# Performance work log

Hardware: AMD Instinct MI355X
Metric: run time of the kernel (lower is better)

Reference implementation:

```python
import jax, jax.numpy as jnp
import numpy as np

B, D, NT, NZ = 16384, 64, 128, 2048


def setup_inputs() -> dict:
    key = jax.random.key(0)
    ks = jax.random.split(key, 5)
    return {
        "t": jax.random.uniform(ks[0], (1,), dtype=jnp.float32),
        "z": jax.random.normal(ks[1], (B, D), dtype=jnp.float32),
        "logp_z": jnp.zeros((B, 1), jnp.float32),
        "centres_z": jax.random.normal(ks[2], (NZ, D), dtype=jnp.float32),
        "log_sigmas_z": jnp.zeros((NZ,), jnp.float32),
        "centres_t": jax.random.normal(ks[3], (NT, 1), dtype=jnp.float32),
        "log_sigmas_t": jnp.zeros((NT,), jnp.float32),
        "W": 0.01 * jax.random.normal(ks[4], (D, NT, NZ + 1), dtype=jnp.float32),
    }


def _gauss(r):
    return jnp.exp(-r * r)


def _forward(t, z, centres_z, log_sigmas_z, centres_t, log_sigmas_t, W):
    # time RBF features Phi_t: (NT,)
    r_t = jnp.abs(t.reshape(1, 1) - centres_t.reshape(1, -1)) / jnp.exp(log_sigmas_t)
    phi_t = _gauss(r_t).reshape(-1)
    W_t = jnp.einsum('dij,i->dj', W, phi_t)  # (D, NZ+1)
    Wz, bias = W_t[:, :-1], W_t[:, -1]       # bias comes from the appended ones column
    # z RBF features via squared-distance identity (avoids [B,NZ,D] blowup)
    sq = (jnp.sum(z * z, axis=1, keepdims=True)
          + jnp.sum(centres_z * centres_z, axis=1)[None, :]
          - 2.0 * z @ centres_z.T)
    sq = jnp.maximum(sq, 0.0)                 # (B, NZ) squared distances
    inv_s2 = jnp.exp(-2.0 * log_sigmas_z)     # 1/sigma_j^2, (NZ,)
    phi_z = jnp.exp(-sq * inv_s2)             # gaussian(||z-c_j||/s_j), (B, NZ)
    dz_dt = phi_z @ Wz.T + bias               # (B, D)
    # exact Jacobian trace for gaussian basis:
    #   d phi_j / d z_i = -2 * phi_j * (z_i - c_{j,i}) / s_j^2
    #   tr(J)_b = sum_j phi_{b,j} * inv_s2_j * (-2) * (sum_i Wz[i,j] z_{b,i} - sum_i Wz[i,j] c_{j,i})
    q = jnp.einsum('dj,jd->j', Wz, centres_z)  # (NZ,)
    trace = -2.0 * jnp.sum(phi_z * inv_s2 * (z @ Wz - q), axis=1)  # (B,)
    dlogp_z_dt = -trace[:, None]               # (B, 1)
    return dz_dt, dlogp_z_dt


def reference(t, z, logp_z, centres_z, log_sigmas_z, centres_t, log_sigmas_t, W):
    return _forward(t, z, centres_z, log_sigmas_z, centres_t, log_sigmas_t, W)
```

## Files before the change

kernel.cpp:

```cpp
#include <hip/hip_runtime.h>
#include <math.h>

typedef unsigned int uint;
typedef unsigned short ushort;
typedef __attribute__((ext_vector_type(8))) short short8;
typedef __attribute__((ext_vector_type(4))) float f32x4;

#define BB  16384
#define DD  64
#define NT_ 128
#define NZ_ 2048
#define NJ_ 2049

#define BIAS_OFF 0
#define SCS_OFF  64
#define ZB0_OFF  8256
#define ZB1_OFF  270400
#define CZ0_OFF  532544
#define CZ1_OFF  565312
#define WZT0_OFF 598080
#define WZT1_OFF 630848
#define WZBP_OFF 663616
#define PART_OFF 729152

__device__ __forceinline__ ushort f2b(float x) {
  uint u = __float_as_uint(x);
  uint r = (u + 0x7FFFu + ((u >> 16) & 1u)) >> 16;
  return (ushort)r;
}
__device__ __forceinline__ ushort f2b_tr(float x) {
  return (ushort)(__float_as_uint(x) >> 16);
}
__device__ __forceinline__ float b2f(ushort h) {
  return __uint_as_float(((uint)h) << 16);
}

__global__ __launch_bounds__(256) void k_wt1(
    const float* __restrict__ t, const float* __restrict__ ct,
    const float* __restrict__ lst, const float* __restrict__ W,
    float* __restrict__ part)
{
  __shared__ float ph[32];
  int tx = threadIdx.x;
  int d  = blockIdx.y;
  int ic = blockIdx.z;
  if (tx < 32) {
    int i = ic * 32 + tx;
    float r = fabsf(t[0] - ct[i]) * __expf(-lst[i]);
    ph[tx] = __expf(-r * r);
  }
  __syncthreads();
  int j = blockIdx.x * 256 + tx;
  if (j >= NJ_) return;
  const float* Wp = W + (size_t)d * NT_ * NJ_ + (size_t)(ic * 32) * NJ_ + j;
  float acc = 0.f;
#pragma unroll
  for (int k = 0; k < 32; ++k) acc += Wp[(size_t)k * NJ_] * ph[k];
  part[((size_t)ic * 64 + d) * NJ_ + j] = acc;
}

__global__ __launch_bounds__(256) void k_prep2(
    const float* __restrict__ part, const float* __restrict__ cz,
    const float* __restrict__ lsz,
    float* __restrict__ bias, float4* __restrict__ scs,
    ushort* __restrict__ czb0, ushort* __restrict__ czb1,
    ushort* __restrict__ wzt0, ushort* __restrict__ wzt1,
    ushort* __restrict__ wzbp)
{
  __shared__ float wt[64][9];
  int tid = threadIdx.x;
  int cb0 = blockIdx.x * 8;
#pragma unroll
  for (int h = 0; h < 2; ++h) {
    int f = h * 256 + tid;
    int d = f >> 3, c = f & 7;
    size_t idx = (size_t)d * NJ_ + cb0 + c;
    float s = part[idx] + part[(size_t)64 * NJ_ + idx]
            + part[(size_t)128 * NJ_ + idx] + part[(size_t)192 * NJ_ + idx];
    wt[d][c] = s;
    int cg = cb0 + c;
    wzbp[((size_t)(cg >> 5) * 64 + d) * 32 + (cg & 31)] = f2b(s);
  }
  if (blockIdx.x == 0 && tid < 64) {
    size_t idx = (size_t)tid * NJ_ + 2048;
    bias[tid] = part[idx] + part[(size_t)64 * NJ_ + idx]
              + part[(size_t)128 * NJ_ + idx] + part[(size_t)192 * NJ_ + idx];
  }
  __syncthreads();
  int cl = tid >> 5;
  int k  = tid & 31;
  int c  = cb0 + cl;
  float cv0 = cz[(size_t)c * DD + k];
  float cv1 = cz[(size_t)c * DD + 32 + k];
  czb0[(size_t)c * 32 + k] = f2b(cv0);
  czb1[(size_t)c * 32 + k] = f2b(cv1);
  float w0 = wt[k][cl], w1 = wt[32 + k][cl];
  wzt0[(size_t)c * 32 + k] = f2b(w0);
  wzt1[(size_t)c * 32 + k] = f2b(w1);
  float ca = cv0 * cv0 + cv1 * cv1;
  float qa = w0 * cv0 + w1 * cv1;
  qa += __shfl_xor(qa, 1);  ca += __shfl_xor(ca, 1);
  qa += __shfl_xor(qa, 2);  ca += __shfl_xor(ca, 2);
  qa += __shfl_xor(qa, 4);  ca += __shfl_xor(ca, 4);
  qa += __shfl_xor(qa, 8);  ca += __shfl_xor(ca, 8);
  qa += __shfl_xor(qa, 16); ca += __shfl_xor(ca, 16);
  if (k == 0) scs[c] = make_float4(ca, __expf(-2.f * lsz[c]), qa, 0.f);
}

__global__ __launch_bounds__(256) void k_zbp(
    const float* __restrict__ z, ushort* __restrict__ zb0, ushort* __restrict__ zb1)
{
  int g = blockIdx.x * 256 + threadIdx.x;
  int r = g >> 3, seg = g & 7;
  const float4* zp = (const float4*)(z + (size_t)r * DD + seg * 8);
  float4 v0 = zp[0], v1 = zp[1];
  short8 o;
  o[0] = (short)f2b(v0.x); o[1] = (short)f2b(v0.y);
  o[2] = (short)f2b(v0.z); o[3] = (short)f2b(v0.w);
  o[4] = (short)f2b(v1.x); o[5] = (short)f2b(v1.y);
  o[6] = (short)f2b(v1.z); o[7] = (short)f2b(v1.w);
  ushort* dst = (seg < 4 ? zb0 : zb1) + (size_t)r * 32 + (seg & 3) * 8;
  *(short8*)dst = o;
}

#define PH_LD 40

__global__ __launch_bounds__(256) void k_fused(
    const ushort* __restrict__ zb0, const ushort* __restrict__ zb1,
    const ushort* __restrict__ czb0, const ushort* __restrict__ czb1,
    const ushort* __restrict__ wzt0, const ushort* __restrict__ wzt1,
    const ushort* __restrict__ wzbp,
    const float4* __restrict__ scs, const float* __restrict__ bias,
    float* __restrict__ out)
{
  __shared__ char smem[10240];
  __shared__ float dlr[4][32];
  ushort* phs = (ushort*)smem;
  float*  eps = (float*)smem;

  int tid  = threadIdx.x;
  int ws   = tid >> 6;
  int lane = tid & 63;
  int lrow = lane & 15, quad = lane >> 4;
  int b0 = blockIdx.x * 32;

  short8 a[2][2];
#pragma unroll
  for (int mt = 0; mt < 2; ++mt) {
    size_t ro = (size_t)(b0 + mt * 16 + lrow) * 32 + quad * 8;
    a[mt][0] = *(const short8*)(zb0 + ro);
    a[mt][1] = *(const short8*)(zb1 + ro);
  }
  float zzr[2][4];
#pragma unroll
  for (int mt = 0; mt < 2; ++mt) {
    float p = 0.f;
#pragma unroll
    for (int k = 0; k < 8; ++k) {
      float v0 = b2f((ushort)a[mt][0][k]), v1 = b2f((ushort)a[mt][1][k]);
      p += v0 * v0 + v1 * v1;
    }
    p += __shfl_xor(p, 16);
    p += __shfl_xor(p, 32);
#pragma unroll
    for (int i = 0; i < 4; ++i) zzr[mt][i] = __shfl(p, quad * 4 + i);
  }

  f32x4 acc[2][4];
#pragma unroll
  for (int mt = 0; mt < 2; ++mt)
#pragma unroll
    for (int nt = 0; nt < 4; ++nt) acc[mt][nt] = (f32x4){0.f, 0.f, 0.f, 0.f};
  float dl[2][4] = {{0.f}};

  const f32x4 zero = (f32x4){0.f, 0.f, 0.f, 0.f};
  int cbase = ws * 512;
  int pbase = ws * 32 * PH_LD;
  for (int cc0 = 0; cc0 < 512; cc0 += 32) {
    int c0 = cbase + cc0;
#pragma unroll
    for (int nt = 0; nt < 2; ++nt) {
      int cg = c0 + nt * 16 + lrow;
      size_t ro = (size_t)cg * 32 + quad * 8;
      short8 bc0 = *(const short8*)(czb0 + ro);
      short8 bc1 = *(const short8*)(czb1 + ro);
      short8 bw0 = *(const short8*)(wzt0 + ro);
      short8 bw1 = *(const short8*)(wzt1 + ro);
      float4 sc = scs[cg];
#pragma unroll
      for (int mt = 0; mt < 2; ++mt) {
        f32x4 d1 = __builtin_amdgcn_mfma_f32_16x16x32_bf16(a[mt][0], bc0, zero, 0, 0, 0);
        d1       = __builtin_amdgcn_mfma_f32_16x16x32_bf16(a[mt][1], bc1, d1,   0, 0, 0);
        f32x4 d2 = __builtin_amdgcn_mfma_f32_16x16x32_bf16(a[mt][0], bw0, zero, 0, 0, 0);
        d2       = __builtin_amdgcn_mfma_f32_16x16x32_bf16(a[mt][1], bw1, d2,   0, 0, 0);
#pragma unroll
        for (int i = 0; i < 4; ++i) {
          float s = zzr[mt][i] + sc.x - 2.f * d1[i];
          s = fmaxf(s, 0.f);
          float p = __expf(-s * sc.y);
          dl[mt][i] += p * sc.y * (d2[i] - sc.z);
          phs[pbase + (mt * 16 + quad * 4 + i) * PH_LD + nt * 16 + lrow] = f2b_tr(p);
        }
      }
    }
    short8 ap0 = *(const short8*)&phs[pbase + lrow * PH_LD + quad * 8];
    short8 ap1 = *(const short8*)&phs[pbase + (16 + lrow) * PH_LD + quad * 8];
    size_t cb = (size_t)(c0 >> 5) * 64 * 32;
#pragma unroll
    for (int nt = 0; nt < 4; ++nt) {
      short8 bb = *(const short8*)(wzbp + cb + (size_t)(nt * 16 + lrow) * 32 + quad * 8);
      acc[0][nt] = __builtin_amdgcn_mfma_f32_16x16x32_bf16(ap0, bb, acc[0][nt], 0, 0, 0);
      acc[1][nt] = __builtin_amdgcn_mfma_f32_16x16x32_bf16(ap1, bb, acc[1][nt], 0, 0, 0);
    }
  }

#pragma unroll
  for (int mt = 0; mt < 2; ++mt)
#pragma unroll
    for (int i = 0; i < 4; ++i) {
      float v = dl[mt][i];
      v += __shfl_xor(v, 1);
      v += __shfl_xor(v, 2);
      v += __shfl_xor(v, 4);
      v += __shfl_xor(v, 8);
      if (lrow == 0) dlr[ws][mt * 16 + quad * 4 + i] = v;
    }

  for (int s = 0; s < 4; ++s) {
    __syncthreads();
    if (ws == s) {
#pragma unroll
      for (int mt = 0; mt < 2; ++mt)
#pragma unroll
        for (int nt = 0; nt < 4; ++nt)
#pragma unroll
          for (int i = 0; i < 4; ++i) {
            int r = mt * 16 + quad * 4 + i;
            int d = nt * 16 + lrow;
            if (s == 0) eps[r * 68 + d] = acc[mt][nt][i];
            else        eps[r * 68 + d] += acc[mt][nt][i];
          }
    }
  }
  __syncthreads();

  {
    int r = tid >> 3, d0 = (tid & 7) * 8;
    float4 e0 = *(const float4*)&eps[r * 68 + d0];
    float4 e1 = *(const float4*)&eps[r * 68 + d0 + 4];
    float4 bv0 = *(const float4*)&bias[d0];
    float4 bv1 = *(const float4*)&bias[d0 + 4];
    float4 o0, o1;
    o0.x = e0.x + bv0.x; o0.y = e0.y + bv0.y; o0.z = e0.z + bv0.z; o0.w = e0.w + bv0.w;
    o1.x = e1.x + bv1.x; o1.y = e1.y + bv1.y; o1.z = e1.z + bv1.z; o1.w = e1.w + bv1.w;
    *(float4*)&out[(size_t)(b0 + r) * DD + d0]     = o0;
    *(float4*)&out[(size_t)(b0 + r) * DD + d0 + 4] = o1;
  }
  if (tid < 32) {
    float s = dlr[0][tid] + dlr[1][tid] + dlr[2][tid] + dlr[3][tid];
    out[(size_t)BB * DD + b0 + tid] = 2.f * s;
  }
}

extern "C" void kernel_launch(void* const* d_in, const int* in_sizes, int n_in,
                              void* d_out, int out_size, void* d_ws, size_t ws_size,
                              hipStream_t stream)
{
  const float* t   = (const float*)d_in[0];
  const float* z   = (const float*)d_in[1];
  const float* cz  = (const float*)d_in[3];
  const float* lsz = (const float*)d_in[4];
  const float* ct  = (const float*)d_in[5];
  const float* lst = (const float*)d_in[6];
  const float* W   = (const float*)d_in[7];
  float* out = (float*)d_out;
  float* ws  = (float*)d_ws;

  float*  bias = ws + BIAS_OFF;
  float4* scs  = (float4*)(ws + SCS_OFF);
  ushort* zb0  = (ushort*)(ws + ZB0_OFF);
  ushort* zb1  = (ushort*)(ws + ZB1_OFF);
  ushort* czb0 = (ushort*)(ws + CZ0_OFF);
  ushort* czb1 = (ushort*)(ws + CZ1_OFF);
  ushort* wzt0 = (ushort*)(ws + WZT0_OFF);
  ushort* wzt1 = (ushort*)(ws + WZT1_OFF);
  ushort* wzbp = (ushort*)(ws + WZBP_OFF);
  float*  part = ws + PART_OFF;

  k_wt1<<<dim3(9, 64, 4), 256, 0, stream>>>(t, ct, lst, W, part);
  k_prep2<<<dim3(256), 256, 0, stream>>>(part, cz, lsz, bias, scs,
                                         czb0, czb1, wzt0, wzt1, wzbp);
  k_zbp<<<dim3(512), 256, 0, stream>>>(z, zb0, zb1);
  k_fused<<<dim3(BB / 32), 256, 0, stream>>>(zb0, zb1, czb0, czb1, wzt0, wzt1,
                                             wzbp, scs, bias, out);
}
```

Baseline: 145.9 us.

## Fuse z bf16 conversion into main kernel and split centres across eight waves

Removes the separate z-to-bf16 packing kernel and its workspace buffer by loading fp32 z directly in the fused kernel and converting in registers. The fused kernel now uses 512 threads per block, with each of eight waves covering 256 centres instead of four waves covering 512. Shared memory for the partial-sum reduction doubles, and the serialized cross-wave reduction grows to eight steps. This trades one launch and a global round-trip for more in-block reduction work and redundant z conversion per wave.

New measurement: 159.8 us. 1.1x slower.

```diff
diff --git a/kernel.cpp b/kernel.cpp
--- a/kernel.cpp
+++ b/kernel.cpp
@@ -14,14 +14,12 @@
 
 #define BIAS_OFF 0
 #define SCS_OFF  64
-#define ZB0_OFF  8256
-#define ZB1_OFF  270400
-#define CZ0_OFF  532544
-#define CZ1_OFF  565312
-#define WZT0_OFF 598080
-#define WZT1_OFF 630848
-#define WZBP_OFF 663616
-#define PART_OFF 729152
+#define CZ0_OFF  8256
+#define CZ1_OFF  41024
+#define WZT0_OFF 73792
+#define WZT1_OFF 106560
+#define WZBP_OFF 139328
+#define PART_OFF 204864
 
 __device__ __forceinline__ ushort f2b(float x) {
   uint u = __float_as_uint(x);
@@ -107,39 +105,23 @@
   if (k == 0) scs[c] = make_float4(ca, __expf(-2.f * lsz[c]), qa, 0.f);
 }
 
-__global__ __launch_bounds__(256) void k_zbp(
-    const float* __restrict__ z, ushort* __restrict__ zb0, ushort* __restrict__ zb1)
-{
-  int g = blockIdx.x * 256 + threadIdx.x;
-  int r = g >> 3, seg = g & 7;
-  const float4* zp = (const float4*)(z + (size_t)r * DD + seg * 8);
-  float4 v0 = zp[0], v1 = zp[1];
-  short8 o;
-  o[0] = (short)f2b(v0.x); o[1] = (short)f2b(v0.y);
-  o[2] = (short)f2b(v0.z); o[3] = (short)f2b(v0.w);
-  o[4] = (short)f2b(v1.x); o[5] = (short)f2b(v1.y);
-  o[6] = (short)f2b(v1.z); o[7] = (short)f2b(v1.w);
-  ushort* dst = (seg < 4 ? zb0 : zb1) + (size_t)r * 32 + (seg & 3) * 8;
-  *(short8*)dst = o;
-}
-
 #define PH_LD 40
 
-__global__ __launch_bounds__(256) void k_fused(
-    const ushort* __restrict__ zb0, const ushort* __restrict__ zb1,
+__global__ __launch_bounds__(512) void k_fused(
+    const float* __restrict__ z,
     const ushort* __restrict__ czb0, const ushort* __restrict__ czb1,
     const ushort* __restrict__ wzt0, const ushort* __restrict__ wzt1,
     const ushort* __restrict__ wzbp,
     const float4* __restrict__ scs, const float* __restrict__ bias,
     float* __restrict__ out)
 {
-  __shared__ char smem[10240];
-  __shared__ float dlr[4][32];
+  __shared__ char smem[20480];
+  __shared__ float dlr[8][32];
   ushort* phs = (ushort*)smem;
   float*  eps = (float*)smem;
 
   int tid  = threadIdx.x;
-  int ws   = tid >> 6;
+  int wv   = tid >> 6;
   int lane = tid & 63;
   int lrow = lane & 15, quad = lane >> 4;
   int b0 = blockIdx.x * 32;
@@ -147,9 +129,18 @@
   short8 a[2][2];
 #pragma unroll
   for (int mt = 0; mt < 2; ++mt) {
-    size_t ro = (size_t)(b0 + mt * 16 + lrow) * 32 + quad * 8;
-    a[mt][0] = *(const short8*)(zb0 + ro);
-    a[mt][1] = *(const short8*)(zb1 + ro);
+    const float* zr = z + (size_t)(b0 + mt * 16 + lrow) * DD;
+#pragma unroll
+    for (int hf = 0; hf < 2; ++hf) {
+      float4 u0 = *(const float4*)(zr + hf * 32 + quad * 8);
+      float4 u1 = *(const float4*)(zr + hf * 32 + quad * 8 + 4);
+      short8 o;
+      o[0] = (short)f2b(u0.x); o[1] = (short)f2b(u0.y);
+      o[2] = (short)f2b(u0.z); o[3] = (short)f2b(u0.w);
+      o[4] = (short)f2b(u1.x); o[5] = (short)f2b(u1.y);
+      o[6] = (short)f2b(u1.z); o[7] = (short)f2b(u1.w);
+      a[mt][hf] = o;
+    }
   }
   float zzr[2][4];
 #pragma unroll
@@ -174,9 +165,9 @@
   float dl[2][4] = {{0.f}};
 
   const f32x4 zero = (f32x4){0.f, 0.f, 0.f, 0.f};
-  int cbase = ws * 512;
-  int pbase = ws * 32 * PH_LD;
-  for (int cc0 = 0; cc0 < 512; cc0 += 32) {
+  int cbase = wv * 256;
+  int pbase = wv * 32 * PH_LD;
+  for (int cc0 = 0; cc0 < 256; cc0 += 32) {
     int c0 = cbase + cc0;
 #pragma unroll
     for (int nt = 0; nt < 2; ++nt) {
@@ -223,12 +214,12 @@
       v += __shfl_xor(v, 2);
       v += __shfl_xor(v, 4);
       v += __shfl_xor(v, 8);
-      if (lrow == 0) dlr[ws][mt * 16 + quad * 4 + i] = v;
-    }
-
-  for (int s = 0; s < 4; ++s) {
+      if (lrow == 0) dlr[wv][mt * 16 + quad * 4 + i] = v;
+    }
+
+  for (int s = 0; s < 8; ++s) {
     __syncthreads();
-    if (ws == s) {
+    if (wv == s) {
 #pragma unroll
       for (int mt = 0; mt < 2; ++mt)
 #pragma unroll
@@ -245,19 +236,17 @@
   __syncthreads();
 
   {
-    int r = tid >> 3, d0 = (tid & 7) * 8;
-    float4 e0 = *(const float4*)&eps[r * 68 + d0];
-    float4 e1 = *(const float4*)&eps[r * 68 + d0 + 4];
-    float4 bv0 = *(const float4*)&bias[d0];
-    float4 bv1 = *(const float4*)&bias[d0 + 4];
-    float4 o0, o1;
-    o0.x = e0.x + bv0.x; o0.y = e0.y + bv0.y; o0.z = e0.z + bv0.z; o0.w = e0.w + bv0.w;
-    o1.x = e1.x + bv1.x; o1.y = e1.y + bv1.y; o1.z = e1.z + bv1.z; o1.w = e1.w + bv1.w;
-    *(float4*)&out[(size_t)(b0 + r) * DD + d0]     = o0;
-    *(float4*)&out[(size_t)(b0 + r) * DD + d0 + 4] = o1;
+    int r = tid >> 4, d0 = (tid & 15) * 4;
+    float4 e  = *(const float4*)&eps[r * 68 + d0];
+    float4 bv = *(const float4*)&bias[d0];
+    float4 o;
+    o.x = e.x + bv.x; o.y = e.y + bv.y; o.z = e.z + bv.z; o.w = e.w + bv.w;
+    *(float4*)&out[(size_t)(b0 + r) * DD + d0] = o;
   }
   if (tid < 32) {
-    float s = dlr[0][tid] + dlr[1][tid] + dlr[2][tid] + dlr[3][tid];
+    float s = 0.f;
+#pragma unroll
+    for (int k = 0; k < 8; ++k) s += dlr[k][tid];
     out[(size_t)BB * DD + b0 + tid] = 2.f * s;
   }
 }
@@ -278,8 +267,6 @@
 
   float*  bias = ws + BIAS_OFF;
   float4* scs  = (float4*)(ws + SCS_OFF);
-  ushort* zb0  = (ushort*)(ws + ZB0_OFF);
-  ushort* zb1  = (ushort*)(ws + ZB1_OFF);
   ushort* czb0 = (ushort*)(ws + CZ0_OFF);
   ushort* czb1 = (ushort*)(ws + CZ1_OFF);
   ushort* wzt0 = (ushort*)(ws + WZT0_OFF);
@@ -290,7 +277,6 @@
   k_wt1<<<dim3(9, 64, 4), 256, 0, stream>>>(t, ct, lst, W, part);
   k_prep2<<<dim3(256), 256, 0, stream>>>(part, cz, lsz, bias, scs,
                                          czb0, czb1, wzt0, wzt1, wzbp);
-  k_zbp<<<dim3(512), 256, 0, stream>>>(z, zb0, zb1);
-  k_fused<<<dim3(BB / 32), 256, 0, stream>>>(zb0, zb1, czb0, czb1, wzt0, wzt1,
+  k_fused<<<dim3(BB / 32), 512, 0, stream>>>(z, czb0, czb1, wzt0, wzt1,
                                              wzbp, scs, bias, out);
 }
```
